# Kernel tuning notes

Hardware: AMD Instinct MI355X
Metric: run time of the kernel (lower is better)

## Reference

```python
import jax, jax.numpy as jnp
import numpy as np


def setup_inputs() -> dict:
    key = jax.random.key(0)
    k1, k2 = jax.random.split(key)
    B, D, F = 16, 512, 1500
    Q, C = 8, 1024
    latents = jax.random.normal(k1, (B, D, F), dtype=jnp.float32)
    # torch init: uniform(-1/size, 1/size)
    codebooks = jax.random.uniform(k2, (Q, C, D), dtype=jnp.float32,
                                   minval=-1.0 / C, maxval=1.0 / C)
    return {"latents": latents, "codebooks": codebooks}


def _rvq(latents, codebooks):
    B, D, F = latents.shape
    Q = codebooks.shape[0]

    def stage(residual, cb):
        # residual: [B, D, F]; cb: [C, D]
        flat = residual.transpose(0, 2, 1).reshape(-1, D)  # [N, D]
        # squared L2 distances via GEMM expansion
        dists = (jnp.sum(flat * flat, axis=1, keepdims=True)
                 - 2.0 * flat @ cb.T
                 + jnp.sum(cb * cb, axis=1))  # [N, C]
        idx = jnp.argmin(dists, axis=1)  # [N]
        q = cb[idx].reshape(B, F, D).transpose(0, 2, 1)  # [B, D, F]
        commit = jnp.mean((residual - jax.lax.stop_gradient(q)) ** 2)
        cb_loss = jnp.mean((q - jax.lax.stop_gradient(residual)) ** 2)
        new_res = residual - jax.lax.stop_gradient(q)
        return new_res, (q, idx.reshape(B, F), commit, cb_loss)

    _, (qs, codes, commits, cb_losses) = jax.lax.scan(stage, latents, codebooks)
    quantized_sum = jnp.sum(qs, axis=0)  # [B, D, F]
    # straight-through estimator
    quantized = latents + jax.lax.stop_gradient(quantized_sum - latents)
    commitment_loss = jnp.sum(commits) / Q
    codebook_loss = jnp.sum(cb_losses) / Q
    codes = jnp.transpose(codes, (1, 0, 2))  # [B, Q, F]
    return quantized, codes, commitment_loss, codebook_loss


def reference(latents, codebooks):
    return _rvq(latents, codebooks)
```

## Files before the change

kernel.cpp:

```cpp
#include <hip/hip_runtime.h>
#include <hip/hip_fp16.h>

#define B_ 16
#define D_ 512
#define F_ 1500
#define N_ (B_*F_)
#define Q_ 8
#define C_ 1024

constexpr int NBLK  = (N_ + 255) / 256;
constexpr int FB_  = (F_ + 31) / 32;
constexpr int TILES_ = B_ * 16 * FB_;
constexpr int SBLK_ = N_ / 64;

typedef __attribute__((ext_vector_type(8))) short bf16x8;
typedef __attribute__((ext_vector_type(4))) short bf16x4;
typedef __attribute__((ext_vector_type(4))) float f32x4;

__device__ __forceinline__ short f2bf(float f) {
    unsigned u = __float_as_uint(f);
    u += 0x7FFFu + ((u >> 16) & 1u);
    return (short)(u >> 16);
}
__device__ __forceinline__ float h2f(unsigned short u) {
    __half_raw r; r.x = u; return __half2float(__half(r));
}
__device__ __forceinline__ unsigned short f2h(float f) {
    __half h = __float2half(f);
    return __half_as_ushort(h);
}

__global__ __launch_bounds__(256) void k_initT(const float* __restrict__ lat,
                                               float* __restrict__ resT,
                                               short* __restrict__ resbf) {
    __shared__ float tile[32][33];
    const int t = threadIdx.x;
    const int row = t >> 3, q4 = t & 7;
    for (int bi = blockIdx.x; bi < TILES_; bi += 1024) {
        int fb = bi % FB_, rem = bi / FB_;
        int db = rem & 15, b = rem >> 4;
        int f0 = fb * 32, d0 = db * 32;
        {
            int fbase = f0 + 4 * q4;
            const float* lp = lat + ((size_t)b * D_ + d0 + row) * F_ + fbase;
            if (fbase + 3 < F_) {
                float4 v = *(const float4*)lp;
                tile[row][4*q4+0] = v.x; tile[row][4*q4+1] = v.y;
                tile[row][4*q4+2] = v.z; tile[row][4*q4+3] = v.w;
            } else {
#pragma unroll
                for (int k = 0; k < 4; ++k)
                    tile[row][4*q4+k] = (fbase + k < F_) ? lp[k] : 0.0f;
            }
        }
        __syncthreads();
        {
            int f = f0 + row;
            if (f < F_) {
                float4 v;
                v.x = tile[4*q4+0][row]; v.y = tile[4*q4+1][row];
                v.z = tile[4*q4+2][row]; v.w = tile[4*q4+3][row];
                size_t o = ((size_t)(b * F_ + f)) * D_ + d0 + 4 * q4;
                *(float4*)(resT + o) = v;
                bf16x4 s;
                s[0] = f2bf(v.x); s[1] = f2bf(v.y); s[2] = f2bf(v.z); s[3] = f2bf(v.w);
                *(bf16x4*)(resbf + o) = s;
            }
        }
        __syncthreads();
    }
}

__global__ void k_cbh(const float* __restrict__ cb, short* __restrict__ cbh) {
    for (int g = blockIdx.x * 256 + threadIdx.x; g < Q_ * C_ * D_ / 8; g += 512 * 256) {
        size_t base = (size_t)g * 8;
        float4 a = *(const float4*)(cb + base);
        float4 b = *(const float4*)(cb + base + 4);
        bf16x8 o;
        o[0]=f2bf(a.x); o[1]=f2bf(a.y); o[2]=f2bf(a.z); o[3]=f2bf(a.w);
        o[4]=f2bf(b.x); o[5]=f2bf(b.y); o[6]=f2bf(b.z); o[7]=f2bf(b.w);
        *(bf16x8*)(cbh + base) = o;
    }
}

__global__ void k_cbnormP(const float* __restrict__ cb, float* __restrict__ Hq) {
#pragma clang fp contract(off)
    int wid = blockIdx.x * 256 + threadIdx.x;
    const float* p = cb + (size_t)wid * D_;
    float L[4];
#pragma unroll
    for (int l = 0; l < 4; ++l) {
        const float* pl = p + l * 128;
        float r[8];
#pragma unroll
        for (int j = 0; j < 8; ++j) { float x = pl[j]; r[j] = x * x; }
        for (int i = 8; i < 128; i += 8) {
#pragma unroll
            for (int j = 0; j < 8; ++j) { float x = pl[i + j]; r[j] = r[j] + x * x; }
        }
        L[l] = ((r[0] + r[1]) + (r[2] + r[3])) + ((r[4] + r[5]) + (r[6] + r[7]));
    }
    Hq[wid] = (L[0] + L[1]) + (L[2] + L[3]);
}

__global__ void k_rownorm4(const float* __restrict__ resT, float* __restrict__ Sp) {
#pragma clang fp contract(off)
    int n = blockIdx.x * 256 + threadIdx.x;
    if (n >= N_) return;
#pragma unroll
    for (int l = 0; l < 4; ++l) {
        const float* p = resT + (size_t)n * D_ + l * 128;
        float r[8];
#pragma unroll
        for (int j = 0; j < 8; ++j) { float x = p[j]; r[j] = x * x; }
        for (int i = 8; i < 128; i += 8) {
#pragma unroll
            for (int j = 0; j < 8; ++j) { float x = p[i + j]; r[j] = r[j] + x * x; }
        }
        Sp[(size_t)l * N_ + n] = ((r[0] + r[1]) + (r[2] + r[3])) + ((r[4] + r[5]) + (r[6] + r[7]));
    }
}

#define LSTR 80
__global__ __launch_bounds__(256) void k_stage(
        const short* __restrict__ cbh, float* __restrict__ resT,
        short* __restrict__ resbf, const float* __restrict__ cb,
        const float* __restrict__ Hq, float* __restrict__ Sp,
        int* __restrict__ codes, double* __restrict__ part, int q) {
#pragma clang fp contract(off)
    __shared__ short xh[64 * LSTR];
    __shared__ short ch[128 * LSTR];
    __shared__ float smin[64][2];
    __shared__ float bminG[64];
    __shared__ unsigned lcnt[64];
    __shared__ unsigned slots[64][16];
    __shared__ unsigned witems[1024];
    __shared__ unsigned long long rkeyL[64];
    __shared__ int fbrows[64];
    __shared__ int codeL[64];
    __shared__ unsigned wcnt_s, fbcnt_s;

    const int t = threadIdx.x, l = t & 63, w = t >> 6;
    const int wr = w >> 1, wc = w & 1;
    const int n0 = blockIdx.x * 64;
    const int nn = t >> 3, d8 = t & 7;
    const short* cbhq = cbh + (size_t)q * C_ * D_;
    const float* Hqq = Hq + (size_t)q * C_;
    const float* cbq = cb + (size_t)q * ((size_t)C_ * D_);

    if (t < 64) { bminG[t] = 3.4e38f; lcnt[t] = 0; rkeyL[t] = ~0ull; }
    if (t == 0) { wcnt_s = 0; fbcnt_s = 0; }

    bf16x8 rxa, rxb, rc[4];
    {
        rxa = *(const bf16x8*)(resbf + (size_t)(n0 + nn) * D_ + d8 * 8);
        rxb = *(const bf16x8*)(resbf + (size_t)(n0 + 32 + nn) * D_ + d8 * 8);
#pragma unroll
        for (int p = 0; p < 4; ++p)
            rc[p] = *(const bf16x8*)(cbhq + (size_t)(32 * p + nn) * D_ + d8 * 8);
    }

    for (int c0 = 0; c0 < C_; c0 += 128) {
        f32x4 acc[2][4];
#pragma unroll
        for (int i = 0; i < 2; ++i)
#pragma unroll
            for (int j = 0; j < 4; ++j) { acc[i][j][0]=0.f; acc[i][j][1]=0.f; acc[i][j][2]=0.f; acc[i][j][3]=0.f; }

        for (int kc = 0; kc < D_; kc += 64) {
            __syncthreads();
            *(bf16x8*)(&xh[nn * LSTR + d8 * 8]) = rxa;
            *(bf16x8*)(&xh[(32 + nn) * LSTR + d8 * 8]) = rxb;
#pragma unroll
            for (int p = 0; p < 4; ++p)
                *(bf16x8*)(&ch[(32 * p + nn) * LSTR + d8 * 8]) = rc[p];
            __syncthreads();

            {
                int nkc = kc + 64, nc0 = c0;
                if (nkc == D_) { nkc = 0; nc0 = c0 + 128; }
                if (nc0 < C_) {
                    rxa = *(const bf16x8*)(resbf + (size_t)(n0 + nn) * D_ + nkc + d8 * 8);
                    rxb = *(const bf16x8*)(resbf + (size_t)(n0 + 32 + nn) * D_ + nkc + d8 * 8);
#pragma unroll
                    for (int p = 0; p < 4; ++p)
                        rc[p] = *(const bf16x8*)(cbhq + (size_t)(nc0 + 32 * p + nn) * D_ + nkc + d8 * 8);
                }
            }

#pragma unroll
            for (int kf = 0; kf < 2; ++kf) {
                const int ko = kf * 32 + (l >> 4) * 8;
                bf16x8 ah[2], bh[4];
#pragma unroll
                for (int i = 0; i < 2; ++i)
                    ah[i] = *(const bf16x8*)(&xh[(wr * 32 + i * 16 + (l & 15)) * LSTR + ko]);
#pragma unroll
                for (int j = 0; j < 4; ++j)
                    bh[j] = *(const bf16x8*)(&ch[(wc * 64 + j * 16 + (l & 15)) * LSTR + ko]);
#pragma unroll
                for (int i = 0; i < 2; ++i)
#pragma unroll
                    for (int j = 0; j < 4; ++j)
                        acc[i][j] = __builtin_amdgcn_mfma_f32_16x16x32_bf16(ah[i], bh[j], acc[i][j], 0, 0, 0);
            }
        }

        float hv[4];
#pragma unroll
        for (int j = 0; j < 4; ++j) hv[j] = Hqq[c0 + wc * 64 + j * 16 + (l & 15)];

#pragma unroll
        for (int i = 0; i < 2; ++i)
#pragma unroll
            for (int r = 0; r < 4; ++r) {
                float vm = hv[0] - 2.0f * acc[i][0][r];
#pragma unroll
                for (int j = 1; j < 4; ++j) vm = fminf(vm, hv[j] - 2.0f * acc[i][j][r]);
                vm = fminf(vm, __shfl_xor(vm, 1, 64));
                vm = fminf(vm, __shfl_xor(vm, 2, 64));
                vm = fminf(vm, __shfl_xor(vm, 4, 64));
                vm = fminf(vm, __shfl_xor(vm, 8, 64));
                if ((l & 15) == 0) smin[wr * 32 + i * 16 + (l >> 4) * 4 + r][wc] = vm;
            }
        __syncthreads();
        if (t < 64) bminG[t] = fminf(bminG[t], fminf(smin[t][0], smin[t][1]));
        __syncthreads();
#pragma unroll
        for (int i = 0; i < 2; ++i)
#pragma unroll
            for (int j = 0; j < 4; ++j)
#pragma unroll
                for (int r = 0; r < 4; ++r) {
                    int row = wr * 32 + i * 16 + (l >> 4) * 4 + r;
                    float v = hv[j] - 2.0f * acc[i][j][r];
                    if (v <= bminG[row] + 1.6e-3f) {
                        unsigned pos = atomicAdd(&lcnt[row], 1u);
                        if (pos < 16) {
                            unsigned c = (unsigned)(c0 + wc * 64 + j * 16 + (l & 15));
                            slots[row][pos] = ((unsigned)f2h(v) << 16) | c;
                        }
                    }
                }
    }
    __syncthreads();

    if (t < 64) {
        float thr = bminG[t] + 1.5e-3f;
        unsigned lc = lcnt[t];
        if (lc > 16u) {
            unsigned fp = atomicAdd(&fbcnt_s, 1u);
            fbrows[fp] = t;
        } else {
            int cnt = 0, c1 = -1;
            for (unsigned s = 0; s < lc; ++s) {
                unsigned e = slots[t][s];
                if (h2f((unsigned short)(e >> 16)) <= thr) { ++cnt; if (cnt == 1) c1 = (int)(e & 0x3FFu); }
            }
            if (cnt == 1) {
                codeL[t] = c1;
            } else {
                codeL[t] = -1;
                for (unsigned s = 0; s < lc; ++s) {
                    unsigned e = slots[t][s];
                    if (h2f((unsigned short)(e >> 16)) <= thr) {
                        unsigned pos = atomicAdd(&wcnt_s, 1u);
                        witems[pos] = ((unsigned)t << 10) | (e & 0x3FFu);
                    }
                }
            }
        }
    }
    __syncthreads();

    {
        unsigned wn = wcnt_s;
        for (unsigned i = t; i < wn; i += 256) {
            unsigned e = witems[i];
            int lr = (int)(e >> 10), c = (int)(e & 0x3FFu);
            int n = n0 + lr;
            float S = (Sp[n] + Sp[N_ + n]) + (Sp[2 * N_ + n] + Sp[3 * N_ + n]);
            const float* xr = resT + (size_t)n * D_;
            const float* cr = cbq + (size_t)c * D_;
            float A = 0.0f;
#pragma unroll 8
            for (int d = 0; d < D_; ++d) A = fmaf(xr[d], cr[d], A);
            float v = (S - 2.0f * A) + Hqq[c];
            unsigned long long key = ((unsigned long long)__float_as_uint(v) << 32) | (unsigned)c;
            atomicMin(&rkeyL[lr], key);
        }
    }
    __syncthreads();
    if (t < 64 && codeL[t] < 0) codeL[t] = (int)(rkeyL[t] & 0x3FFull);

    {
        unsigned fn = fbcnt_s;
        for (unsigned fi = w; fi < fn; fi += 4) {
            int lr = fbrows[fi];
            int n = n0 + lr;
            float S = (Sp[n] + Sp[N_ + n]) + (Sp[2 * N_ + n] + Sp[3 * N_ + n]);
            const float4* xr4 = (const float4*)(resT + (size_t)n * D_);
            float mn = 3.4e38f;
            for (int rep = 0; rep < 16; ++rep) {
                int c = l + rep * 64;
                const float4* cr4 = (const float4*)(cbq + (size_t)c * D_);
                float a0 = 0.f, a1 = 0.f, a2 = 0.f, a3 = 0.f;
#pragma unroll 4
                for (int d4 = 0; d4 < 128; ++d4) {
                    float4 xv = xr4[d4], cv = cr4[d4];
                    a0 = fmaf(xv.x, cv.x, a0); a1 = fmaf(xv.y, cv.y, a1);
                    a2 = fmaf(xv.z, cv.z, a2); a3 = fmaf(xv.w, cv.w, a3);
                }
                float v = (S - 2.0f * ((a0 + a1) + (a2 + a3))) + Hqq[c];
                mn = fminf(mn, v);
            }
            for (int off = 32; off; off >>= 1) mn = fminf(mn, __shfl_xor(mn, off, 64));
            const float thr2 = mn + 6e-4f;
            float bv = 3.4e38f; int bc = 0x7fffffff;
            const float* xr = resT + (size_t)n * D_;
            for (int rep = 0; rep < 16; ++rep) {
                int c = l + rep * 64;
                const float4* cr4 = (const float4*)(cbq + (size_t)c * D_);
                float a0 = 0.f, a1 = 0.f, a2 = 0.f, a3 = 0.f;
#pragma unroll 4
                for (int d4 = 0; d4 < 128; ++d4) {
                    float4 xv = xr4[d4], cv = cr4[d4];
                    a0 = fmaf(xv.x, cv.x, a0); a1 = fmaf(xv.y, cv.y, a1);
                    a2 = fmaf(xv.z, cv.z, a2); a3 = fmaf(xv.w, cv.w, a3);
                }
                float vap = (S - 2.0f * ((a0 + a1) + (a2 + a3))) + Hqq[c];
                if (vap <= thr2) {
                    const float* cr = cbq + (size_t)c * D_;
                    float A = 0.0f;
#pragma unroll 8
                    for (int d = 0; d < D_; ++d) A = fmaf(xr[d], cr[d], A);
                    float v = (S - 2.0f * A) + Hqq[c];
                    if (v < bv || (v == bv && c < bc)) { bv = v; bc = c; }
                }
            }
            for (int off = 32; off; off >>= 1) {
                float ov = __shfl_xor(bv, off, 64);
                int oc = __shfl_xor(bc, off, 64);
                if (ov < bv || (ov == bv && oc < bc)) { bv = ov; bc = oc; }
            }
            if (l == 0) codeL[lr] = bc;
        }
    }
    __syncthreads();
    if (t < 64) codes[(size_t)q * N_ + n0 + t] = codeL[t];

    float L = 0.0f;
    {
        int lr = t >> 2, seg = t & 3;
        int n = n0 + lr;
        int idx = codeL[lr];
        const float4* cr4 = (const float4*)(cb + ((size_t)q * C_ + idx) * D_ + seg * 128);
        float4* rp4 = (float4*)(resT + (size_t)n * D_ + seg * 128);
        short* rb = resbf + (size_t)n * D_ + seg * 128;
        float r8[8];
#pragma unroll
        for (int k = 0; k < 16; ++k) {
            float4 a = rp4[2*k], b = rp4[2*k+1];
            float4 ca = cr4[2*k], cb2 = cr4[2*k+1];
            float v0 = a.x - ca.x, v1 = a.y - ca.y, v2 = a.z - ca.z, v3 = a.w - ca.w;
            float v4 = b.x - cb2.x, v5 = b.y - cb2.y, v6 = b.z - cb2.z, v7 = b.w - cb2.w;
            rp4[2*k]   = float4{v0, v1, v2, v3};
            rp4[2*k+1] = float4{v4, v5, v6, v7};
            bf16x8 o;
            o[0]=f2bf(v0); o[1]=f2bf(v1); o[2]=f2bf(v2); o[3]=f2bf(v3);
            o[4]=f2bf(v4); o[5]=f2bf(v5); o[6]=f2bf(v6); o[7]=f2bf(v7);
            *(bf16x8*)(rb + 8*k) = o;
            if (k == 0) {
                r8[0]=v0*v0; r8[1]=v1*v1; r8[2]=v2*v2; r8[3]=v3*v3;
                r8[4]=v4*v4; r8[5]=v5*v5; r8[6]=v6*v6; r8[7]=v7*v7;
            } else {
                r8[0]=r8[0]+v0*v0; r8[1]=r8[1]+v1*v1; r8[2]=r8[2]+v2*v2; r8[3]=r8[3]+v3*v3;
                r8[4]=r8[4]+v4*v4; r8[5]=r8[5]+v5*v5; r8[6]=r8[6]+v6*v6; r8[7]=r8[7]+v7*v7;
            }
        }
        L = ((r8[0] + r8[1]) + (r8[2] + r8[3])) + ((r8[4] + r8[5]) + (r8[6] + r8[7]));
        Sp[(size_t)seg * N_ + n] = L;
    }
    double s = (double)L;
#pragma unroll
    for (int off = 32; off; off >>= 1) s += __shfl_down(s, off, 64);
    __shared__ double sred[4];
    int lane = threadIdx.x & 63, wv = threadIdx.x >> 6;
    if (lane == 0) sred[wv] = s;
    __syncthreads();
    if (threadIdx.x == 0)
        part[(size_t)q * SBLK_ + blockIdx.x] = sred[0] + sred[1] + sred[2] + sred[3];
}

__global__ __launch_bounds__(256) void k_out0T(const float* __restrict__ lat,
                                               const float* __restrict__ resT,
                                               float* __restrict__ out) {
    __shared__ float tile[32][33];
    const int t = threadIdx.x;
    const int row = t >> 3, q4 = t & 7;
    for (int bi = blockIdx.x; bi < TILES_; bi += 1024) {
        int fb = bi % FB_, rem = bi / FB_;
        int db = rem & 15, b = rem >> 4;
        int f0 = fb * 32, d0 = db * 32;
        {
            int f = f0 + row;
            if (f < F_) {
                float4 v = *(const float4*)(resT + ((size_t)(b * F_ + f)) * D_ + d0 + 4 * q4);
                tile[4*q4+0][row] = v.x; tile[4*q4+1][row] = v.y;
                tile[4*q4+2][row] = v.z; tile[4*q4+3][row] = v.w;
            }
        }
        __syncthreads();
        {
            int fbase = f0 + 4 * q4;
            size_t o = ((size_t)b * D_ + d0 + row) * F_ + fbase;
            if (fbase + 3 < F_) {
                float4 lv = *(const float4*)(lat + o);
                float4 v;
                v.x = lv.x - tile[row][4*q4+0]; v.y = lv.y - tile[row][4*q4+1];
                v.z = lv.z - tile[row][4*q4+2]; v.w = lv.w - tile[row][4*q4+3];
                *(float4*)(out + o) = v;
            } else {
#pragma unroll
                for (int k = 0; k < 4; ++k)
                    if (fbase + k < F_) out[o + k] = lat[o + k] - tile[row][4*q4+k];
            }
        }
        __syncthreads();
    }
}

__global__ void k_codes(const int* __restrict__ codes, float* __restrict__ out1) {
    int bi = blockIdx.x;
    int q = bi & 7, b = bi >> 3;
    for (int f = threadIdx.x; f < F_; f += 256)
        out1[(size_t)bi * F_ + f] = (float)codes[(size_t)q * N_ + (size_t)b * F_ + f];
}

__global__ void k_loss(const double* __restrict__ part, float* __restrict__ out2) {
    double s = 0.0;
    for (int i = threadIdx.x; i < Q_ * SBLK_; i += 256) s += part[i];
#pragma unroll
    for (int off = 32; off; off >>= 1) s += __shfl_down(s, off, 64);
    __shared__ double red[4];
    int lane = threadIdx.x & 63, wv = threadIdx.x >> 6;
    if (lane == 0) red[wv] = s;
    __syncthreads();
    if (threadIdx.x == 0) {
        double tot = red[0] + red[1] + red[2] + red[3];
        float val = (float)(tot / ((double)Q_ * (double)B_ * (double)D_ * (double)F_));
        out2[0] = val;
        out2[1] = val;
    }
}

extern "C" void kernel_launch(void* const* d_in, const int* in_sizes, int n_in,
                              void* d_out, int out_size, void* d_ws, size_t ws_size,
                              hipStream_t stream) {
    const float* lat = (const float*)d_in[0];
    const float* cb  = (const float*)d_in[1];
    char* ws = (char*)d_ws;
    float*  resT  = (float*)(ws);
    short*  resbf = (short*)(ws + 49283072);
    short*  cbh   = (short*)(ws + 73924608);
    int*    codes = (int*)(ws + 82313216);
    float*  Hq    = (float*)(ws + 83081216);
    float*  Sp    = (float*)(ws + 83113984);
    double* part  = (double*)(ws + 83497984);
    float* out = (float*)d_out;

    hipLaunchKernelGGL(k_initT,    dim3(1024), dim3(256), 0, stream, lat, resT, resbf);
    hipLaunchKernelGGL(k_cbh,      dim3(512), dim3(256), 0, stream, cb, cbh);
    hipLaunchKernelGGL(k_cbnormP,  dim3(Q_ * C_ / 256), dim3(256), 0, stream, cb, Hq);
    hipLaunchKernelGGL(k_rownorm4, dim3(NBLK), dim3(256), 0, stream, resT, Sp);

    for (int q = 0; q < Q_; ++q) {
        hipLaunchKernelGGL(k_stage, dim3(SBLK_), dim3(256), 0, stream,
                           cbh, resT, resbf, cb, Hq, Sp, codes, part, q);
    }

    hipLaunchKernelGGL(k_out0T, dim3(1024), dim3(256), 0, stream, lat, resT, out);
    hipLaunchKernelGGL(k_codes, dim3(B_ * Q_), dim3(256), 0, stream, codes, out + 12288000);
    hipLaunchKernelGGL(k_loss,  dim3(1), dim3(256), 0, stream, part, out + 12480000);
}
```

Measured before the change: 1.154 ms.

## Drop LDS staging in stage GEMM; 8 waves read operands directly from global

```diff
diff --git a/kernel.cpp b/kernel.cpp
--- a/kernel.cpp
+++ b/kernel.cpp
@@ -121,16 +121,13 @@
     }
 }
 
-#define LSTR 80
-__global__ __launch_bounds__(256) void k_stage(
+__global__ __launch_bounds__(512) void k_stage(
         const short* __restrict__ cbh, float* __restrict__ resT,
         short* __restrict__ resbf, const float* __restrict__ cb,
         const float* __restrict__ Hq, float* __restrict__ Sp,
         int* __restrict__ codes, double* __restrict__ part, int q) {
 #pragma clang fp contract(off)
-    __shared__ short xh[64 * LSTR];
-    __shared__ short ch[128 * LSTR];
-    __shared__ float smin[64][2];
+    __shared__ float smin[64][8];
     __shared__ float bminG[64];
     __shared__ unsigned lcnt[64];
     __shared__ unsigned slots[64][16];
@@ -141,77 +138,77 @@
     __shared__ unsigned wcnt_s, fbcnt_s;
 
     const int t = threadIdx.x, l = t & 63, w = t >> 6;
-    const int wr = w >> 1, wc = w & 1;
+    const int lr16 = l & 15, lk = l >> 4;
     const int n0 = blockIdx.x * 64;
-    const int nn = t >> 3, d8 = t & 7;
     const short* cbhq = cbh + (size_t)q * C_ * D_;
     const float* Hqq = Hq + (size_t)q * C_;
     const float* cbq = cb + (size_t)q * ((size_t)C_ * D_);
 
     if (t < 64) { bminG[t] = 3.4e38f; lcnt[t] = 0; rkeyL[t] = ~0ull; }
     if (t == 0) { wcnt_s = 0; fbcnt_s = 0; }
-
-    bf16x8 rxa, rxb, rc[4];
-    {
-        rxa = *(const bf16x8*)(resbf + (size_t)(n0 + nn) * D_ + d8 * 8);
-        rxb = *(const bf16x8*)(resbf + (size_t)(n0 + 32 + nn) * D_ + d8 * 8);
-#pragma unroll
-        for (int p = 0; p < 4; ++p)
-            rc[p] = *(const bf16x8*)(cbhq + (size_t)(32 * p + nn) * D_ + d8 * 8);
-    }
-
-    for (int c0 = 0; c0 < C_; c0 += 128) {
-        f32x4 acc[2][4];
-#pragma unroll
-        for (int i = 0; i < 2; ++i)
+    __syncthreads();
+
+    const short* arow[4];
+#pragma unroll
+    for (int i = 0; i < 4; ++i)
+        arow[i] = resbf + (size_t)(n0 + i * 16 + lr16) * D_ + lk * 8;
+
+    for (int s = 0; s < 2; ++s) {
+        const int cbase = s * 512 + w * 64;
+        const short* brow[4];
+#pragma unroll
+        for (int j = 0; j < 4; ++j)
+            brow[j] = cbhq + (size_t)(cbase + j * 16 + lr16) * D_ + lk * 8;
+
+        f32x4 acc[4][4];
+#pragma unroll
+        for (int i = 0; i < 4; ++i)
 #pragma unroll
             for (int j = 0; j < 4; ++j) { acc[i][j][0]=0.f; acc[i][j][1]=0.f; acc[i][j][2]=0.f; acc[i][j][3]=0.f; }
 
-        for (int kc = 0; kc < D_; kc += 64) {
-            __syncthreads();
-            *(bf16x8*)(&xh[nn * LSTR + d8 * 8]) = rxa;
-            *(bf16x8*)(&xh[(32 + nn) * LSTR + d8 * 8]) = rxb;
-#pragma unroll
-            for (int p = 0; p < 4; ++p)
-                *(bf16x8*)(&ch[(32 * p + nn) * LSTR + d8 * 8]) = rc[p];
-            __syncthreads();
-
-            {
-                int nkc = kc + 64, nc0 = c0;
-                if (nkc == D_) { nkc = 0; nc0 = c0 + 128; }
-                if (nc0 < C_) {
-                    rxa = *(const bf16x8*)(resbf + (size_t)(n0 + nn) * D_ + nkc + d8 * 8);
-                    rxb = *(const bf16x8*)(resbf + (size_t)(n0 + 32 + nn) * D_ + nkc + d8 * 8);
-#pragma unroll
-                    for (int p = 0; p < 4; ++p)
-                        rc[p] = *(const bf16x8*)(cbhq + (size_t)(nc0 + 32 * p + nn) * D_ + nkc + d8 * 8);
-                }
-            }
-
-#pragma unroll
-            for (int kf = 0; kf < 2; ++kf) {
-                const int ko = kf * 32 + (l >> 4) * 8;
-                bf16x8 ah[2], bh[4];
-#pragma unroll
-                for (int i = 0; i < 2; ++i)
-                    ah[i] = *(const bf16x8*)(&xh[(wr * 32 + i * 16 + (l & 15)) * LSTR + ko]);
+        bf16x8 a0[4], b0[4], a1[4], b1[4];
+#pragma unroll
+        for (int i = 0; i < 4; ++i) { a0[i] = *(const bf16x8*)(arow[i]); b0[i] = *(const bf16x8*)(brow[i]); }
+#pragma unroll 4
+        for (int kc = 0; kc < 512; kc += 64) {
+#pragma unroll
+            for (int i = 0; i < 4; ++i) {
+                a1[i] = *(const bf16x8*)(arow[i] + kc + 32);
+                b1[i] = *(const bf16x8*)(brow[i] + kc + 32);
+            }
+#pragma unroll
+            for (int i = 0; i < 4; ++i)
 #pragma unroll
                 for (int j = 0; j < 4; ++j)
-                    bh[j] = *(const bf16x8*)(&ch[(wc * 64 + j * 16 + (l & 15)) * LSTR + ko]);
-#pragma unroll
-                for (int i = 0; i < 2; ++i)
-#pragma unroll
-                    for (int j = 0; j < 4; ++j)
-                        acc[i][j] = __builtin_amdgcn_mfma_f32_16x16x32_bf16(ah[i], bh[j], acc[i][j], 0, 0, 0);
-            }
+                    acc[i][j] = __builtin_amdgcn_mfma_f32_16x16x32_bf16(a0[i], b0[j], acc[i][j], 0, 0, 0);
+            if (kc + 64 < 512) {
+#pragma unroll
+                for (int i = 0; i < 4; ++i) {
+                    a0[i] = *(const bf16x8*)(arow[i] + kc + 64);
+                    b0[i] = *(const bf16x8*)(brow[i] + kc + 64);
+                }
+            } else if (s == 0) {
+#pragma unroll
+                for (int i = 0; i < 4; ++i)
+                    b0[i] = *(const bf16x8*)(cbhq + (size_t)(512 + w * 64 + i * 16 + lr16) * D_ + lk * 8);
+            }
+#pragma unroll
+            for (int i = 0; i < 4; ++i)
+#pragma unroll
+                for (int j = 0; j < 4; ++j)
+                    acc[i][j] = __builtin_amdgcn_mfma_f32_16x16x32_bf16(a1[i], b1[j], acc[i][j], 0, 0, 0);
+        }
+        if (s == 0) {
+#pragma unroll
+            for (int i = 0; i < 4; ++i) a0[i] = *(const bf16x8*)(arow[i]);
         }
 
         float hv[4];
 #pragma unroll
-        for (int j = 0; j < 4; ++j) hv[j] = Hqq[c0 + wc * 64 + j * 16 + (l & 15)];
-
-#pragma unroll
-        for (int i = 0; i < 2; ++i)
+        for (int j = 0; j < 4; ++j) hv[j] = Hqq[cbase + j * 16 + lr16];
+
+#pragma unroll
+        for (int i = 0; i < 4; ++i)
 #pragma unroll
             for (int r = 0; r < 4; ++r) {
                 float vm = hv[0] - 2.0f * acc[i][0][r];
@@ -221,23 +218,27 @@
                 vm = fminf(vm, __shfl_xor(vm, 2, 64));
                 vm = fminf(vm, __shfl_xor(vm, 4, 64));
                 vm = fminf(vm, __shfl_xor(vm, 8, 64));
-                if ((l & 15) == 0) smin[wr * 32 + i * 16 + (l >> 4) * 4 + r][wc] = vm;
-            }
-        __syncthreads();
-        if (t < 64) bminG[t] = fminf(bminG[t], fminf(smin[t][0], smin[t][1]));
-        __syncthreads();
-#pragma unroll
-        for (int i = 0; i < 2; ++i)
+                if (lr16 == 0) smin[i * 16 + lk * 4 + r][w] = vm;
+            }
+        __syncthreads();
+        if (t < 64) {
+            float m2 = fminf(fminf(smin[t][0], smin[t][1]), fminf(smin[t][2], smin[t][3]));
+            m2 = fminf(m2, fminf(fminf(smin[t][4], smin[t][5]), fminf(smin[t][6], smin[t][7])));
+            bminG[t] = fminf(bminG[t], m2);
+        }
+        __syncthreads();
+#pragma unroll
+        for (int i = 0; i < 4; ++i)
 #pragma unroll
             for (int j = 0; j < 4; ++j)
 #pragma unroll
                 for (int r = 0; r < 4; ++r) {
-                    int row = wr * 32 + i * 16 + (l >> 4) * 4 + r;
+                    int row = i * 16 + lk * 4 + r;
                     float v = hv[j] - 2.0f * acc[i][j][r];
                     if (v <= bminG[row] + 1.6e-3f) {
                         unsigned pos = atomicAdd(&lcnt[row], 1u);
                         if (pos < 16) {
-                            unsigned c = (unsigned)(c0 + wc * 64 + j * 16 + (l & 15));
+                            unsigned c = (unsigned)(cbase + j * 16 + lr16);
                             slots[row][pos] = ((unsigned)f2h(v) << 16) | c;
                         }
                     }
@@ -275,7 +276,7 @@
 
     {
         unsigned wn = wcnt_s;
-        for (unsigned i = t; i < wn; i += 256) {
+        for (unsigned i = t; i < wn; i += 512) {
             unsigned e = witems[i];
             int lr = (int)(e >> 10), c = (int)(e & 0x3FFu);
             int n = n0 + lr;
@@ -295,7 +296,7 @@
 
     {
         unsigned fn = fbcnt_s;
-        for (unsigned fi = w; fi < fn; fi += 4) {
+        for (unsigned fi = w; fi < fn; fi += 8) {
             int lr = fbrows[fi];
             int n = n0 + lr;
             float S = (Sp[n] + Sp[N_ + n]) + (Sp[2 * N_ + n] + Sp[3 * N_ + n]);
@@ -350,7 +351,7 @@
     if (t < 64) codes[(size_t)q * N_ + n0 + t] = codeL[t];
 
     float L = 0.0f;
-    {
+    if (t < 256) {
         int lr = t >> 2, seg = t & 3;
         int n = n0 + lr;
         int idx = codeL[lr];
@@ -384,12 +385,13 @@
     double s = (double)L;
 #pragma unroll
     for (int off = 32; off; off >>= 1) s += __shfl_down(s, off, 64);
-    __shared__ double sred[4];
+    __shared__ double sred[8];
     int lane = threadIdx.x & 63, wv = threadIdx.x >> 6;
     if (lane == 0) sred[wv] = s;
     __syncthreads();
     if (threadIdx.x == 0)
-        part[(size_t)q * SBLK_ + blockIdx.x] = sred[0] + sred[1] + sred[2] + sred[3];
+        part[(size_t)q * SBLK_ + blockIdx.x] = ((sred[0] + sred[1]) + (sred[2] + sred[3]))
+                                            + ((sred[4] + sred[5]) + (sred[6] + sred[7]));
 }
 
 __global__ __launch_bounds__(256) void k_out0T(const float* __restrict__ lat,
@@ -475,7 +477,7 @@
     hipLaunchKernelGGL(k_rownorm4, dim3(NBLK), dim3(256), 0, stream, resT, Sp);
 
     for (int q = 0; q < Q_; ++q) {
-        hipLaunchKernelGGL(k_stage, dim3(SBLK_), dim3(256), 0, stream,
+        hipLaunchKernelGGL(k_stage, dim3(SBLK_), dim3(512), 0, stream,
                            cbh, resT, resbf, cb, Hq, Sp, codes, part, q);
     }
 
```

Measured after the change: 1.763 ms. +52.8%, slower.
